# Kernel optimization log

Measured on AMD Instinct MI355X. Metric: run time of the kernel, lower is better.

Reference implementation:

```python
import jax, jax.numpy as jnp
import numpy as np

B, N, D_MODEL, H = 4, 4096, 1024, 16
DEPTH = D_MODEL // H
EPS_Z = 1e-9
EPS_LN = 1e-6


def setup_inputs() -> dict:
    key = jax.random.key(0)
    ks = jax.random.split(key, 12)
    s = 1.0 / np.sqrt(D_MODEL)
    return {
        "query": jax.random.normal(ks[0], (B, N, D_MODEL), jnp.float32),
        "key": jax.random.normal(ks[1], (B, N, D_MODEL), jnp.float32),
        "value": jax.random.normal(ks[2], (B, N, D_MODEL), jnp.float32),
        "Wq": jax.random.normal(ks[3], (D_MODEL, D_MODEL), jnp.float32) * s,
        "bq": jnp.zeros((D_MODEL,), jnp.float32),
        "Wk": jax.random.normal(ks[4], (D_MODEL, D_MODEL), jnp.float32) * s,
        "bk": jnp.zeros((D_MODEL,), jnp.float32),
        "Wv": jax.random.normal(ks[5], (D_MODEL, D_MODEL), jnp.float32) * s,
        "bv": jnp.zeros((D_MODEL,), jnp.float32),
        "Wo": jax.random.normal(ks[6], (D_MODEL, D_MODEL), jnp.float32) * s,
        "bo": jnp.zeros((D_MODEL,), jnp.float32),
        "gamma": jnp.ones((D_MODEL,), jnp.float32),
        "beta": jnp.zeros((D_MODEL,), jnp.float32),
    }


def _split_heads(x):
    # [B, N, d_model] -> [B, H, N, depth]
    b, n, _ = x.shape
    return x.reshape(b, n, H, DEPTH).transpose(0, 2, 1, 3)


def reference(query, key, value, Wq, bq, Wk, bk, Wv, bv, Wo, bo, gamma, beta):
    Q = _split_heads(query @ Wq + bq)
    K = _split_heads(key @ Wk + bk)
    V = _split_heads(value @ Wv + bv)

    Q = jax.nn.elu(Q) + 1.0
    K = jax.nn.elu(K) + 1.0

    # Normalizer: Z[b,h,n] = K[b,h,n,:] . sum_l Q[b,h,l,:]
    q_sum = jnp.sum(Q, axis=2)                          # [B,H,d]
    Z = jnp.einsum('bhnd,bhd->bhn', K, q_sum)[..., None]  # [B,H,N,1]

    # output[b,h,m,e] = sum_l sum_d K[l,d] V[m,d] Q[l,e]
    #                 = sum_d V[m,d] * (sum_l K[l,d] Q[l,e])
    KtQ = jnp.einsum('bhld,bhle->bhde', K, Q)           # [B,H,d,d]
    out = jnp.einsum('bhmd,bhde->bhme', V, KtQ)         # [B,H,N,d]
    out = out / (Z + EPS_Z)

    # combine heads -> [B, N, d_model]
    out = out.transpose(0, 2, 1, 3).reshape(query.shape[0], -1, D_MODEL)
    attn = out @ Wo + bo

    x = query + attn
    mu = jnp.mean(x, axis=-1, keepdims=True)
    var = jnp.mean(jnp.square(x - mu), axis=-1, keepdims=True)
    return (x - mu) * jax.lax.rsqrt(var + EPS_LN) * gamma + beta
```

## Files before the change

kernel.cpp:

```cpp
#include <hip/hip_runtime.h>
#include <hip/hip_bf16.h>


typedef __attribute__((ext_vector_type(8))) short short8;
typedef __attribute__((ext_vector_type(4))) float floatx4;
typedef __attribute__((ext_vector_type(4))) unsigned short ushortx4;
typedef __attribute__((ext_vector_type(8))) unsigned short ushortx8;

#define DEVINL __device__ __forceinline__

DEVINL unsigned short f2bf(float f) {
  unsigned int u = __builtin_bit_cast(unsigned int, f);
  u += 0x7fffu + ((u >> 16) & 1u);
  return (unsigned short)(u >> 16);
}
DEVINL float bf2f(unsigned short h) {
  unsigned int u = ((unsigned int)h) << 16;
  return __builtin_bit_cast(float, u);
}
DEVINL void g2l16(const void* g, void* l) {
  __builtin_amdgcn_global_load_lds((const __attribute__((address_space(1))) void*)g,
                                   (__attribute__((address_space(3))) void*)l, 16, 0, 0);
}

__global__ __launch_bounds__(256) void conv_kernel(const float* __restrict__ in,
                                                   unsigned short* __restrict__ out) {
  const size_t i = ((size_t)blockIdx.x * 256 + threadIdx.x) * 8;
  const float4 a = *(const float4*)(in + i);
  const float4 b = *(const float4*)(in + i + 4);
  ushortx8 o;
  o[0] = f2bf(a.x); o[1] = f2bf(a.y); o[2] = f2bf(a.z); o[3] = f2bf(a.w);
  o[4] = f2bf(b.x); o[5] = f2bf(b.y); o[6] = f2bf(b.z); o[7] = f2bf(b.w);
  *(ushortx8*)(out + i) = o;
}

struct W4 { const float* w[4]; };

__global__ __launch_bounds__(256) void wtrans_kernel(W4 wp, unsigned short* wt) {
  const int z = blockIdx.z;
  const float* W = wp.w[z];
  unsigned short* WT = wt + (size_t)z * 1024 * 1024;
  __shared__ float tile[32][33];
  const int bx = blockIdx.x, by = blockIdx.y;
  const int t = threadIdx.x, r = t >> 5, c = t & 31;
#pragma unroll
  for (int p = 0; p < 4; ++p)
    tile[p * 8 + r][c] = W[(size_t)(by * 32 + p * 8 + r) * 1024 + bx * 32 + c];
  __syncthreads();
#pragma unroll
  for (int p = 0; p < 4; ++p)
    WT[(size_t)(bx * 32 + p * 8 + r) * 1024 + by * 32 + c] = f2bf(tile[c][p * 8 + r]);
}

#define CT_S 136
__global__ __launch_bounds__(256) void gemm_bt_kernel(const unsigned short* __restrict__ A,
                                                      const unsigned short* __restrict__ BT,
                                                      const float* __restrict__ bias,
                                                      unsigned short* __restrict__ C,
                                                      int act, int qsflag, int zflag,
                                                      float* qsum, float* Z,
                                                      int M, int N, int K) {
  const int mb = M >> 7;
  const int id = blockIdx.x;
  const int m0 = (id % mb) * 128;
  const int n0 = (id / mb) * 128;
  __shared__ unsigned short smem[128 * 128];
  unsigned short* lA = smem;
  unsigned short* lB = smem + 8192;
  const int t = threadIdx.x, lane = t & 63, wave = t >> 6;
  const int wm = wave >> 1, wn = wave & 1;

  floatx4 acc[4][4] = {};

  const int srow = lane >> 3;
  const int scol = ((lane & 7) ^ srow) * 8;
  const int rl = lane & 15;
  const int qw = lane >> 4;

  for (int k0 = 0; k0 < K; k0 += 64) {
    __syncthreads();
#pragma unroll
    for (int i = 0; i < 4; ++i) {
      const int c = wave * 4 + i;
      g2l16(BT + (size_t)(n0 + c * 8 + srow) * K + (k0 + scol), (void*)&lB[c * 512]);
      g2l16(A + (size_t)(m0 + c * 8 + srow) * K + (k0 + scol), (void*)&lA[c * 512]);
    }
    __syncthreads();
#pragma unroll
    for (int ks = 0; ks < 2; ++ks) {
      short8 af[4], bfr[4];
#pragma unroll
      for (int mt = 0; mt < 4; ++mt)
        af[mt] = *(const short8*)&lA[(wm * 64 + mt * 16 + rl) * 64 +
                                     (((ks * 4 + qw) ^ (rl & 7)) * 8)];
#pragma unroll
      for (int nt = 0; nt < 4; ++nt)
        bfr[nt] = *(const short8*)&lB[(wn * 64 + nt * 16 + rl) * 64 +
                                      (((ks * 4 + qw) ^ (rl & 7)) * 8)];
#pragma unroll
      for (int mt = 0; mt < 4; ++mt)
#pragma unroll
        for (int nt = 0; nt < 4; ++nt)
          acc[mt][nt] = __builtin_amdgcn_mfma_f32_16x16x32_bf16(af[mt], bfr[nt], acc[mt][nt], 0, 0, 0);
    }
  }

  const int bb = m0 >> 12;
  float cs[4] = {0.f, 0.f, 0.f, 0.f};
  float zp[4][4] = {};
#pragma unroll
  for (int p = 0; p < 2; ++p) {
    __syncthreads();
    if (wm == p) {
#pragma unroll
      for (int nt = 0; nt < 4; ++nt) {
        const int coll = wn * 64 + nt * 16 + (lane & 15);
        const int colg = n0 + coll;
        const float bv = bias[colg];
        float qsv = 0.f;
        if (zflag) qsv = qsum[(bb * 16 + (colg >> 6)) * 64 + (colg & 63)];
#pragma unroll
        for (int mt = 0; mt < 4; ++mt) {
#pragma unroll
          for (int r = 0; r < 4; ++r) {
            const int rowl = mt * 16 + (lane >> 4) * 4 + r;
            float v = acc[mt][nt][r] + bv;
            if (act) v = (v > 0.f) ? (v + 1.f) : __expf(v);
            cs[nt] += v;
            if (zflag) zp[mt][r] += v * qsv;
            smem[rowl * CT_S + coll] = f2bf(v);
          }
        }
      }
    }
    __syncthreads();
    {
      const int cc = (t & 15) * 8;
#pragma unroll
      for (int q = 0; q < 4; ++q) {
        const int row = q * 16 + (t >> 4);
        *(short8*)(C + (size_t)(m0 + p * 64 + row) * N + n0 + cc) =
            *(const short8*)&smem[row * CT_S + cc];
      }
    }
  }
  if (qsflag) {
#pragma unroll
    for (int nt = 0; nt < 4; ++nt) {
      float v = cs[nt];
      v += __shfl_xor(v, 16);
      v += __shfl_xor(v, 32);
      if (lane < 16) {
        const int colg = n0 + wn * 64 + nt * 16 + lane;
        atomicAdd(&qsum[(bb * 16 + (colg >> 6)) * 64 + (colg & 63)], v);
      }
    }
  }
  if (zflag) {
    const int h = (n0 >> 6) + wn;
#pragma unroll
    for (int mt = 0; mt < 4; ++mt) {
#pragma unroll
      for (int r = 0; r < 4; ++r) {
        float v = zp[mt][r];
        v += __shfl_xor(v, 1); v += __shfl_xor(v, 2);
        v += __shfl_xor(v, 4); v += __shfl_xor(v, 8);
        if ((lane & 15) == 0) {
          const int rowg = m0 + wm * 64 + mt * 16 + (lane >> 4) * 4 + r;
          Z[((size_t)(bb * 16 + h)) * 4096 + (rowg & 4095)] = v;
        }
      }
    }
  }
}

#define KTS 136
__global__ __launch_bounds__(256) void ktq_partial_kernel(const unsigned short* Qp,
                                                          const unsigned short* Kp,
                                                          float* part) {
  const int bh = blockIdx.x, b = bh >> 4, h = bh & 15;
  const int s = blockIdx.y;
  const unsigned short* Qh = Qp + (size_t)b * 4096 * 1024 + h * 64;
  const unsigned short* Kh = Kp + (size_t)b * 4096 * 1024 + h * 64;
  __shared__ unsigned short Kt[64 * KTS];
  __shared__ unsigned short Qt[64 * KTS];
  const int t = threadIdx.x, lane = t & 63, wave = t >> 6;
  floatx4 acc[4] = {};
  const int nlb = t >> 3;
  const int dblk = (t & 7) * 8;

  for (int c0 = s * 512; c0 < s * 512 + 512; c0 += 128) {
    __syncthreads();
#pragma unroll
    for (int it = 0; it < 4; ++it) {
      const int nl = it * 32 + nlb;
      const size_t goff = (size_t)(c0 + nl) * 1024 + dblk;
      short8 kv = *(const short8*)(Kh + goff);
      short8 qv = *(const short8*)(Qh + goff);
#pragma unroll
      for (int j = 0; j < 8; ++j) {
        Kt[(dblk + j) * KTS + nl] = (unsigned short)kv[j];
        Qt[(dblk + j) * KTS + nl] = (unsigned short)qv[j];
      }
    }
    __syncthreads();
#pragma unroll
    for (int ks = 0; ks < 4; ++ks) {
      const short8 a = *(const short8*)&Kt[(wave * 16 + (lane & 15)) * KTS + ks * 32 + (lane >> 4) * 8];
#pragma unroll
      for (int et = 0; et < 4; ++et) {
        const short8 bb = *(const short8*)&Qt[(et * 16 + (lane & 15)) * KTS + ks * 32 + (lane >> 4) * 8];
        acc[et] = __builtin_amdgcn_mfma_f32_16x16x32_bf16(a, bb, acc[et], 0, 0, 0);
      }
    }
  }
  float* outp = part + ((size_t)(s * 64 + bh)) * 4096;
#pragma unroll
  for (int et = 0; et < 4; ++et) {
    const int e = et * 16 + (lane & 15);
#pragma unroll
    for (int r = 0; r < 4; ++r) {
      const int d = wave * 16 + (lane >> 4) * 4 + r;
      outp[e * 64 + d] = acc[et][r];
    }
  }
}

__global__ __launch_bounds__(256) void ktq_reduce_kernel(const float* __restrict__ part,
                                                         unsigned short* __restrict__ ktqt) {
  const int bh = blockIdx.x, t = threadIdx.x;
#pragma unroll
  for (int i = 0; i < 16; ++i) {
    const int idx = i * 256 + t;
    float s = 0.f;
#pragma unroll
    for (int sl = 0; sl < 8; ++sl) s += part[((size_t)(sl * 64 + bh)) * 4096 + idx];
    ktqt[(size_t)bh * 4096 + idx] = f2bf(s);
  }
}

#define CTS 72
__global__ __launch_bounds__(256) void stagec_kernel(const unsigned short* Vp,
                                                     const unsigned short* ktqt,
                                                     const float* __restrict__ Z,
                                                     unsigned short* U) {
  const int bh = blockIdx.y, b = bh >> 4, h = bh & 15;
  const int n0 = blockIdx.x * 256;
  __shared__ unsigned short kt_lds[64 * CTS];
  __shared__ float zbuf[256];
  const int t = threadIdx.x, lane = t & 63, wave = t >> 6;

  {
    const unsigned short* src = ktqt + (size_t)bh * 4096;
    const int row = t >> 2, seg = (t & 3) * 16;
    *(short8*)&kt_lds[row * CTS + seg] = *(const short8*)(src + row * 64 + seg);
    *(short8*)&kt_lds[row * CTS + seg + 8] = *(const short8*)(src + row * 64 + seg + 8);
  }
  zbuf[t] = Z[(size_t)bh * 4096 + n0 + t];
  __syncthreads();

  const unsigned short* Vh = Vp + (size_t)b * 4096 * 1024 + h * 64;
  floatx4 acc[4][4] = {};
#pragma unroll
  for (int ks = 0; ks < 2; ++ks) {
    short8 bfr[4];
#pragma unroll
    for (int et = 0; et < 4; ++et)
      bfr[et] = *(const short8*)&kt_lds[(et * 16 + (lane & 15)) * CTS + ks * 32 + (lane >> 4) * 8];
#pragma unroll
    for (int mt = 0; mt < 4; ++mt) {
      const short8 a = *(const short8*)(Vh + (size_t)(n0 + wave * 64 + mt * 16 + (lane & 15)) * 1024 +
                                        ks * 32 + (lane >> 4) * 8);
#pragma unroll
      for (int et = 0; et < 4; ++et)
        acc[mt][et] = __builtin_amdgcn_mfma_f32_16x16x32_bf16(a, bfr[et], acc[mt][et], 0, 0, 0);
    }
  }
#pragma unroll
  for (int mt = 0; mt < 4; ++mt) {
#pragma unroll
    for (int r = 0; r < 4; ++r) {
      const int rl = wave * 64 + mt * 16 + (lane >> 4) * 4 + r;
      const float inv = 1.0f / (zbuf[rl] + 1e-9f);
#pragma unroll
      for (int et = 0; et < 4; ++et) {
        const int e = et * 16 + (lane & 15);
        U[((size_t)b * 4096 + n0 + rl) * 1024 + h * 64 + e] = f2bf(acc[mt][et][r] * inv);
      }
    }
  }
}

__global__ __launch_bounds__(256) void ln_kernel(const float* query, const unsigned short* attn,
                                                 const float* gamma, const float* beta, float* out) {
  const int row = blockIdx.x, t = threadIdx.x;
  const float* qrow = query + (size_t)row * 1024;
  const unsigned short* arow = attn + (size_t)row * 1024;
  const float4 qv = *(const float4*)(qrow + t * 4);
  const ushortx4 av = *(const ushortx4*)(arow + t * 4);
  float x0 = qv.x + bf2f(av.x), x1 = qv.y + bf2f(av.y);
  float x2 = qv.z + bf2f(av.z), x3 = qv.w + bf2f(av.w);
  float s = x0 + x1 + x2 + x3;
  float s2 = x0 * x0 + x1 * x1 + x2 * x2 + x3 * x3;
  for (int off = 32; off > 0; off >>= 1) {
    s += __shfl_down(s, off);
    s2 += __shfl_down(s2, off);
  }
  __shared__ float lred[8];
  if ((t & 63) == 0) { lred[(t >> 6) * 2] = s; lred[(t >> 6) * 2 + 1] = s2; }
  __syncthreads();
  s = lred[0] + lred[2] + lred[4] + lred[6];
  s2 = lred[1] + lred[3] + lred[5] + lred[7];
  const float mu = s * (1.f / 1024.f);
  const float var = s2 * (1.f / 1024.f) - mu * mu;
  const float rstd = rsqrtf(var + 1e-6f);
  float4 o;
  o.x = (x0 - mu) * rstd * gamma[t * 4 + 0] + beta[t * 4 + 0];
  o.y = (x1 - mu) * rstd * gamma[t * 4 + 1] + beta[t * 4 + 1];
  o.z = (x2 - mu) * rstd * gamma[t * 4 + 2] + beta[t * 4 + 2];
  o.w = (x3 - mu) * rstd * gamma[t * 4 + 3] + beta[t * 4 + 3];
  *(float4*)(out + (size_t)row * 1024 + t * 4) = o;
}

extern "C" void kernel_launch(void* const* d_in, const int* in_sizes, int n_in,
                              void* d_out, int out_size, void* d_ws, size_t ws_size,
                              hipStream_t stream) {
  const float* query = (const float*)d_in[0];
  const float* key_  = (const float*)d_in[1];
  const float* value = (const float*)d_in[2];
  const float* Wq = (const float*)d_in[3];
  const float* bq = (const float*)d_in[4];
  const float* Wk = (const float*)d_in[5];
  const float* bk = (const float*)d_in[6];
  const float* Wv = (const float*)d_in[7];
  const float* bv = (const float*)d_in[8];
  const float* Wo = (const float*)d_in[9];
  const float* bo = (const float*)d_in[10];
  const float* gamma = (const float*)d_in[11];
  const float* beta = (const float*)d_in[12];
  float* out = (float*)d_out;

  char* ws = (char*)d_ws;
  unsigned short* abf = (unsigned short*)(ws + 0);
  unsigned short* Qp = (unsigned short*)(ws + 33554432);
  unsigned short* Kp = (unsigned short*)(ws + 67108864);
  unsigned short* Vp = (unsigned short*)(ws + 100663296);
  unsigned short* WT = (unsigned short*)(ws + 134217728);
  float* qsumP = (float*)(ws + 142606336);
  unsigned short* ktqtP = (unsigned short*)(ws + 142606336 + 16384);
  float* Zp = (float*)(ws + 142606336 + 16384 + 524288);
  float* part = (float*)abf;
  unsigned short* U = abf;
  unsigned short* attn = Qp;

  dim3 blk(256);

  W4 w4; w4.w[0] = Wq; w4.w[1] = Wk; w4.w[2] = Wv; w4.w[3] = Wo;
  wtrans_kernel<<<dim3(32, 32, 4), blk, 0, stream>>>(w4, WT);

  hipMemsetAsync(qsumP, 0, 64 * 64 * sizeof(float), stream);

  const int convGrid = 8192;
  const int gemmGrid = 128 * 8;

  conv_kernel<<<convGrid, blk, 0, stream>>>(query, abf);
  gemm_bt_kernel<<<gemmGrid, blk, 0, stream>>>(abf, WT, bq, Qp, 1, 1, 0, qsumP, Zp,
                                               16384, 1024, 1024);

  conv_kernel<<<convGrid, blk, 0, stream>>>(key_, abf);
  gemm_bt_kernel<<<gemmGrid, blk, 0, stream>>>(abf, WT + 1024 * 1024, bk, Kp, 1, 0, 1,
                                               qsumP, Zp, 16384, 1024, 1024);

  conv_kernel<<<convGrid, blk, 0, stream>>>(value, abf);
  gemm_bt_kernel<<<gemmGrid, blk, 0, stream>>>(abf, WT + 2 * 1024 * 1024, bv, Vp, 0, 0, 0,
                                               qsumP, Zp, 16384, 1024, 1024);

  ktq_partial_kernel<<<dim3(64, 8), blk, 0, stream>>>(Qp, Kp, part);
  ktq_reduce_kernel<<<64, blk, 0, stream>>>(part, ktqtP);
  stagec_kernel<<<dim3(16, 64), blk, 0, stream>>>(Vp, ktqtP, Zp, U);

  gemm_bt_kernel<<<gemmGrid, blk, 0, stream>>>(U, WT + 3 * 1024 * 1024, bo, attn, 0, 0, 0,
                                               qsumP, Zp, 16384, 1024, 1024);

  ln_kernel<<<16384, blk, 0, stream>>>(query, attn, gamma, beta, out);
}
```

Before: 558.4 us.

## Rewrite projection GEMM with 256x256 tiles and double-buffered async LDS pipeline

```diff
diff --git a/kernel.cpp b/kernel.cpp
--- a/kernel.cpp
+++ b/kernel.cpp
@@ -52,98 +52,143 @@
     WT[(size_t)(bx * 32 + p * 8 + r) * 1024 + by * 32 + c] = f2bf(tile[c][p * 8 + r]);
 }
 
-#define CT_S 136
-__global__ __launch_bounds__(256) void gemm_bt_kernel(const unsigned short* __restrict__ A,
-                                                      const unsigned short* __restrict__ BT,
-                                                      const float* __restrict__ bias,
-                                                      unsigned short* __restrict__ C,
-                                                      int act, int qsflag, int zflag,
-                                                      float* qsum, float* Z,
-                                                      int M, int N, int K) {
-  const int mb = M >> 7;
+__global__ __launch_bounds__(512, 2) void gemm_bt_kernel(const unsigned short* __restrict__ A,
+                                                         const unsigned short* __restrict__ BT,
+                                                         const float* __restrict__ bias,
+                                                         unsigned short* __restrict__ C,
+                                                         int act, int qsflag, int zflag,
+                                                         float* qsum, float* Z,
+                                                         int M, int N, int K) {
+  const int mb = M >> 8;
   const int id = blockIdx.x;
-  const int m0 = (id % mb) * 128;
-  const int n0 = (id / mb) * 128;
-  __shared__ unsigned short smem[128 * 128];
-  unsigned short* lA = smem;
-  unsigned short* lB = smem + 8192;
+  const int m0 = (id % mb) << 8;
+  const int n0 = (id / mb) << 8;
+  __shared__ unsigned short smem[65536];
   const int t = threadIdx.x, lane = t & 63, wave = t >> 6;
-  const int wm = wave >> 1, wn = wave & 1;
-
-  floatx4 acc[4][4] = {};
-
+  const int wm = wave >> 2, wn = wave & 3;
   const int srow = lane >> 3;
   const int scol = ((lane & 7) ^ srow) * 8;
-  const int rl = lane & 15;
-  const int qw = lane >> 4;
-
-  for (int k0 = 0; k0 < K; k0 += 64) {
-    __syncthreads();
-#pragma unroll
-    for (int i = 0; i < 4; ++i) {
-      const int c = wave * 4 + i;
-      g2l16(BT + (size_t)(n0 + c * 8 + srow) * K + (k0 + scol), (void*)&lB[c * 512]);
-      g2l16(A + (size_t)(m0 + c * 8 + srow) * K + (k0 + scol), (void*)&lA[c * 512]);
-    }
-    __syncthreads();
-#pragma unroll
-    for (int ks = 0; ks < 2; ++ks) {
-      short8 af[4], bfr[4];
-#pragma unroll
-      for (int mt = 0; mt < 4; ++mt)
-        af[mt] = *(const short8*)&lA[(wm * 64 + mt * 16 + rl) * 64 +
-                                     (((ks * 4 + qw) ^ (rl & 7)) * 8)];
-#pragma unroll
-      for (int nt = 0; nt < 4; ++nt)
-        bfr[nt] = *(const short8*)&lB[(wn * 64 + nt * 16 + rl) * 64 +
-                                      (((ks * 4 + qw) ^ (rl & 7)) * 8)];
-#pragma unroll
-      for (int mt = 0; mt < 4; ++mt)
+  const int rl = lane & 15, qw = lane >> 4;
+  const int NT = K >> 6;
+
+  floatx4 acc[8][4] = {};
+
+  const unsigned short* Ag = A + (size_t)m0 * K;
+  const unsigned short* Bg = BT + (size_t)n0 * K;
+
+#define LA(c) (smem + (c) * 32768)
+#define LB(c) (smem + (c) * 32768 + 16384)
+
+  auto STG = [&](unsigned short* Lt, const unsigned short* Gt, int R, int k0) {
+    const int r0 = R + wave * 8;
+    g2l16(Gt + (size_t)(r0 + srow) * K + (k0 + scol), (void*)(Lt + r0 * 64));
+  };
+
+  STG(LB(0), Bg, 0, 0);    STG(LB(0), Bg, 64, 0);
+  STG(LB(0), Bg, 128, 0);  STG(LB(0), Bg, 192, 0);
+  STG(LA(0), Ag, 0, 0);    STG(LA(0), Ag, 128, 0);
+  STG(LA(0), Ag, 64, 0);   STG(LA(0), Ag, 192, 0);
+  STG(LB(1), Bg, 0, 64);   STG(LB(1), Bg, 64, 64);
+  STG(LB(1), Bg, 128, 64); STG(LB(1), Bg, 192, 64);
+  STG(LA(1), Ag, 0, 64);   STG(LA(1), Ag, 128, 64);
+  asm volatile("s_waitcnt vmcnt(6)" ::: "memory");
+  __builtin_amdgcn_s_barrier();
+
+  for (int tk = 0; tk < NT; ++tk) {
+    unsigned short* lAc = LA(tk & 1);
+    unsigned short* lBc = LB(tk & 1);
+    short8 bf[4][2];
+#pragma unroll
+    for (int q = 0; q < 4; ++q) {
+      if (q == 0) {
 #pragma unroll
         for (int nt = 0; nt < 4; ++nt)
-          acc[mt][nt] = __builtin_amdgcn_mfma_f32_16x16x32_bf16(af[mt], bfr[nt], acc[mt][nt], 0, 0, 0);
-    }
-  }
-
+#pragma unroll
+          for (int ks = 0; ks < 2; ++ks)
+            bf[nt][ks] = *(const short8*)&lBc[(wn * 64 + nt * 16 + rl) * 64 +
+                                              (((ks * 4 + qw) ^ (rl & 7)) * 8)];
+      }
+      short8 af[2][2];
+#pragma unroll
+      for (int mt = 0; mt < 2; ++mt)
+#pragma unroll
+        for (int ks = 0; ks < 2; ++ks)
+          af[mt][ks] = *(const short8*)&lAc[(wm * 128 + q * 32 + mt * 16 + rl) * 64 +
+                                            (((ks * 4 + qw) ^ (rl & 7)) * 8)];
+      if (q == 0) {
+        if (tk + 1 < NT) {
+          const int k1 = (tk + 1) << 6;
+          unsigned short* lAn = LA((tk + 1) & 1);
+          STG(lAn, Ag, 64, k1); STG(lAn, Ag, 192, k1);
+        }
+      } else if (q == 1) {
+        if (tk + 2 < NT) { const int k2 = (tk + 2) << 6; STG(lBc, Bg, 0, k2); STG(lBc, Bg, 64, k2); }
+      } else if (q == 2) {
+        if (tk + 2 < NT) { const int k2 = (tk + 2) << 6; STG(lBc, Bg, 128, k2); STG(lBc, Bg, 192, k2); }
+      } else {
+        if (tk + 2 < NT) { const int k2 = (tk + 2) << 6; STG(lAc, Ag, 0, k2); STG(lAc, Ag, 128, k2); }
+      }
+      __builtin_amdgcn_s_barrier();
+      asm volatile("s_waitcnt lgkmcnt(0)" ::: "memory");
+      __builtin_amdgcn_s_setprio(1);
+#pragma unroll
+      for (int ks = 0; ks < 2; ++ks)
+#pragma unroll
+        for (int mt = 0; mt < 2; ++mt)
+#pragma unroll
+          for (int nt = 0; nt < 4; ++nt)
+            acc[q * 2 + mt][nt] = __builtin_amdgcn_mfma_f32_16x16x32_bf16(
+                af[mt][ks], bf[nt][ks], acc[q * 2 + mt][nt], 0, 0, 0);
+      __builtin_amdgcn_s_setprio(0);
+      if (q == 3 && tk + 1 < NT) {
+        if (tk + 1 == NT - 1) asm volatile("s_waitcnt vmcnt(0)" ::: "memory");
+        else                  asm volatile("s_waitcnt vmcnt(6)" ::: "memory");
+      }
+      __builtin_amdgcn_s_barrier();
+    }
+  }
+
+  __syncthreads();
   const int bb = m0 >> 12;
   float cs[4] = {0.f, 0.f, 0.f, 0.f};
-  float zp[4][4] = {};
-#pragma unroll
-  for (int p = 0; p < 2; ++p) {
-    __syncthreads();
-    if (wm == p) {
-#pragma unroll
-      for (int nt = 0; nt < 4; ++nt) {
-        const int coll = wn * 64 + nt * 16 + (lane & 15);
-        const int colg = n0 + coll;
-        const float bv = bias[colg];
-        float qsv = 0.f;
-        if (zflag) qsv = qsum[(bb * 16 + (colg >> 6)) * 64 + (colg & 63)];
-#pragma unroll
-        for (int mt = 0; mt < 4; ++mt) {
-#pragma unroll
-          for (int r = 0; r < 4; ++r) {
-            const int rowl = mt * 16 + (lane >> 4) * 4 + r;
-            float v = acc[mt][nt][r] + bv;
-            if (act) v = (v > 0.f) ? (v + 1.f) : __expf(v);
-            cs[nt] += v;
-            if (zflag) zp[mt][r] += v * qsv;
-            smem[rowl * CT_S + coll] = f2bf(v);
-          }
-        }
-      }
-    }
-    __syncthreads();
-    {
-      const int cc = (t & 15) * 8;
-#pragma unroll
-      for (int q = 0; q < 4; ++q) {
-        const int row = q * 16 + (t >> 4);
-        *(short8*)(C + (size_t)(m0 + p * 64 + row) * N + n0 + cc) =
-            *(const short8*)&smem[row * CT_S + cc];
-      }
-    }
-  }
+  float zacc[8][4];
+#pragma unroll
+  for (int mt = 0; mt < 8; ++mt)
+#pragma unroll
+    for (int r = 0; r < 4; ++r) zacc[mt][r] = 0.f;
+
+#pragma unroll
+  for (int nt = 0; nt < 4; ++nt) {
+    const int coll = wn * 64 + nt * 16 + rl;
+    const int colg = n0 + coll;
+    const float bv = bias[colg];
+    float qsv = 0.f;
+    if (zflag) qsv = qsum[(bb * 16 + (colg >> 6)) * 64 + (colg & 63)];
+    const int chnk = wn * 4 + nt;
+#pragma unroll
+    for (int mt = 0; mt < 8; ++mt) {
+#pragma unroll
+      for (int r = 0; r < 4; ++r) {
+        const int rowl = wm * 128 + mt * 16 + qw * 4 + r;
+        float v = acc[mt][nt][r] + bv;
+        if (act) v = (v > 0.f) ? (v + 1.f) : __expf(v);
+        cs[nt] += v;
+        if (zflag) zacc[mt][r] += v * qsv;
+        smem[rowl * 256 + ((chnk ^ (rowl & 15)) * 16) + rl] = f2bf(v);
+      }
+    }
+  }
+  __syncthreads();
+#pragma unroll
+  for (int i = 0; i < 16; ++i) {
+    const int idx = i * 512 + t;
+    const int row = idx >> 5;
+    const int seg = idx & 31;
+    const int phys = (seg >> 1) ^ (row & 15);
+    *(short8*)(C + (size_t)(m0 + row) * N + n0 + seg * 8) =
+        *(const short8*)&smem[row * 256 + phys * 16 + (seg & 1) * 8];
+  }
+
   if (qsflag) {
 #pragma unroll
     for (int nt = 0; nt < 4; ++nt) {
@@ -159,14 +204,14 @@
   if (zflag) {
     const int h = (n0 >> 6) + wn;
 #pragma unroll
-    for (int mt = 0; mt < 4; ++mt) {
+    for (int mt = 0; mt < 8; ++mt) {
 #pragma unroll
       for (int r = 0; r < 4; ++r) {
-        float v = zp[mt][r];
+        float v = zacc[mt][r];
         v += __shfl_xor(v, 1); v += __shfl_xor(v, 2);
         v += __shfl_xor(v, 4); v += __shfl_xor(v, 8);
         if ((lane & 15) == 0) {
-          const int rowg = m0 + wm * 64 + mt * 16 + (lane >> 4) * 4 + r;
+          const int rowg = m0 + wm * 128 + mt * 16 + qw * 4 + r;
           Z[((size_t)(bb * 16 + h)) * 4096 + (rowg & 4095)] = v;
         }
       }
@@ -354,6 +399,7 @@
   unsigned short* attn = Qp;
 
   dim3 blk(256);
+  dim3 gblk(512);
 
   W4 w4; w4.w[0] = Wq; w4.w[1] = Wk; w4.w[2] = Wv; w4.w[3] = Wo;
   wtrans_kernel<<<dim3(32, 32, 4), blk, 0, stream>>>(w4, WT);
@@ -361,26 +407,26 @@
   hipMemsetAsync(qsumP, 0, 64 * 64 * sizeof(float), stream);
 
   const int convGrid = 8192;
-  const int gemmGrid = 128 * 8;
+  const int gemmGrid = 64 * 4;
 
   conv_kernel<<<convGrid, blk, 0, stream>>>(query, abf);
-  gemm_bt_kernel<<<gemmGrid, blk, 0, stream>>>(abf, WT, bq, Qp, 1, 1, 0, qsumP, Zp,
-                                               16384, 1024, 1024);
+  gemm_bt_kernel<<<gemmGrid, gblk, 0, stream>>>(abf, WT, bq, Qp, 1, 1, 0, qsumP, Zp,
+                                                16384, 1024, 1024);
 
   conv_kernel<<<convGrid, blk, 0, stream>>>(key_, abf);
-  gemm_bt_kernel<<<gemmGrid, blk, 0, stream>>>(abf, WT + 1024 * 1024, bk, Kp, 1, 0, 1,
-                                               qsumP, Zp, 16384, 1024, 1024);
+  gemm_bt_kernel<<<gemmGrid, gblk, 0, stream>>>(abf, WT + 1024 * 1024, bk, Kp, 1, 0, 1,
+                                                qsumP, Zp, 16384, 1024, 1024);
 
   conv_kernel<<<convGrid, blk, 0, stream>>>(value, abf);
-  gemm_bt_kernel<<<gemmGrid, blk, 0, stream>>>(abf, WT + 2 * 1024 * 1024, bv, Vp, 0, 0, 0,
-                                               qsumP, Zp, 16384, 1024, 1024);
+  gemm_bt_kernel<<<gemmGrid, gblk, 0, stream>>>(abf, WT + 2 * 1024 * 1024, bv, Vp, 0, 0, 0,
+                                                qsumP, Zp, 16384, 1024, 1024);
 
   ktq_partial_kernel<<<dim3(64, 8), blk, 0, stream>>>(Qp, Kp, part);
   ktq_reduce_kernel<<<64, blk, 0, stream>>>(part, ktqtP);
   stagec_kernel<<<dim3(16, 64), blk, 0, stream>>>(Vp, ktqtP, Zp, U);
 
-  gemm_bt_kernel<<<gemmGrid, blk, 0, stream>>>(U, WT + 3 * 1024 * 1024, bo, attn, 0, 0, 0,
-                                               qsumP, Zp, 16384, 1024, 1024);
+  gemm_bt_kernel<<<gemmGrid, gblk, 0, stream>>>(U, WT + 3 * 1024 * 1024, bo, attn, 0, 0, 0,
+                                                qsumP, Zp, 16384, 1024, 1024);
 
   ln_kernel<<<16384, blk, 0, stream>>>(query, attn, gamma, beta, out);
 }
```

Result: faster. 498.1 us (-10.8%).
